# Kernel optimization log

Hardware: AMD Instinct MI355X
Metric: run time of the kernel (lower is better)

The kernel has to match this reference:

```python
import jax, jax.numpy as jnp
import numpy as np

NUM_HEADS = 6
WIN = 16
NW = 16   # number of windows sharing one mask (b_ % NW == 0)


def setup_inputs() -> dict:
    key = jax.random.key(0)
    ks = jax.random.split(key, 6)
    b_, n, dim = 256, WIN * WIN, 192
    qkv = jax.random.normal(ks[0], (b_, n, 3 * dim), dtype=jnp.float32)
    rpi = jax.random.randint(ks[1], (n, n), 0, (2 * WIN - 1) * (2 * WIN - 1))
    # additive attention mask per window-group (Swin uses 0 / -100; randn is fine for math)
    mask = jax.random.normal(ks[2], (NW, n, n), dtype=jnp.float32)
    rpb_table = 0.02 * jax.random.normal(ks[3], ((2 * WIN - 1) * (2 * WIN - 1), NUM_HEADS), dtype=jnp.float32)
    proj_w = jax.random.normal(ks[4], (dim, dim), dtype=jnp.float32) * (1.0 / np.sqrt(dim))
    proj_b = jax.random.normal(ks[5], (dim,), dtype=jnp.float32) * 0.01
    return {"qkv": qkv, "rpi": rpi, "mask": mask, "rpb_table": rpb_table,
            "proj_w": proj_w, "proj_b": proj_b}


def reference(qkv, rpi, mask, rpb_table, proj_w, proj_b):
    b_, n, c3 = qkv.shape
    c = c3 // 3
    h = NUM_HEADS
    hd = c // h
    scale = float(hd) ** -0.5
    # (b_, n, 3, h, hd) -> (3, b_, h, n, hd)
    qkv = qkv.reshape(b_, n, 3, h, hd).transpose(2, 0, 3, 1, 4)
    q, k, v = qkv[0] * scale, qkv[1], qkv[2]
    attn = jnp.einsum('bhqd,bhkd->bhqk', q, k)  # [b_, h, n, n]
    # gathered relative position bias: [n, n, h] -> [h, n, n]
    bias = rpb_table[rpi].transpose(2, 0, 1)
    attn = attn + bias[None]
    # add per-window-group mask: [b_//nw, nw, h, n, n]
    nw = mask.shape[0]
    attn = attn.reshape(b_ // nw, nw, h, n, n) + mask[None, :, None]
    attn = attn.reshape(b_, h, n, n)
    attn = jax.nn.softmax(attn, axis=-1)
    x = jnp.einsum('bhqk,bhkd->bhqd', attn, v)  # [b_, h, n, hd]
    x = x.transpose(0, 2, 1, 3).reshape(b_, n, c)
    # nn.Linear: x @ W^T + b
    return x @ proj_w.T + proj_b
```

## Files before the change

### kernel.cpp

```cpp
#include <hip/hip_runtime.h>
#include <hip/hip_bf16.h>

typedef _Float16 f16;
typedef _Float16 f16x2 __attribute__((ext_vector_type(2)));
typedef _Float16 f16x4 __attribute__((ext_vector_type(4)));
typedef _Float16 f16x8 __attribute__((ext_vector_type(8)));
typedef __fp16 h16x2 __attribute__((ext_vector_type(2)));
typedef float f32x4 __attribute__((ext_vector_type(4)));

#define NHEADS 6
#define NTOK 256
#define NWINS 256
#define DIM 192
#define HD 32
#define C3 576
#define LOG2E 1.4426950408889634f
#define SCALE (0.17677669529663687f * LOG2E)

__device__ inline f16x2 pkrtz(float a, float b) {
  h16x2 r = __builtin_amdgcn_cvt_pkrtz(a, b);
  return __builtin_bit_cast(f16x2, r);
}

__global__ __launch_bounds__(256) void prep_cb_kernel(const int* __restrict__ rpi,
                                                      const float* __restrict__ mask,
                                                      const float* __restrict__ rpb,
                                                      f16* __restrict__ cb) {
  int idx = blockIdx.x * 256 + threadIdx.x;
  int rem = idx & 255;
  int q = (idx >> 8) & 255;
  int t = idx >> 16;
  int h = t % 6;
  int mg = t / 6;
  int ktp = rem >> 5;
  int gg = (rem >> 3) & 3;
  int e = rem & 7;
  int k = (2 * ktp + (e >> 2)) * 16 + gg * 4 + (e & 3);
  float v = (rpb[rpi[(q << 8) | k] * 6 + h] + mask[(mg << 16) | (q << 8) | k]) * LOG2E;
  cb[idx] = (f16)v;
}

__global__ __launch_bounds__(256) void prep_w_kernel(const float* __restrict__ w,
                                                     f16* __restrict__ w16) {
  int i = blockIdx.x * 256 + threadIdx.x;
  if (i < DIM * DIM) w16[i] = (f16)w[i];
}

__device__ inline f16x8 q_to_f16(float4 a, float4 b) {
  f16x2 p0 = pkrtz(a.x * SCALE, a.y * SCALE);
  f16x2 p1 = pkrtz(a.z * SCALE, a.w * SCALE);
  f16x2 p2 = pkrtz(b.x * SCALE, b.y * SCALE);
  f16x2 p3 = pkrtz(b.z * SCALE, b.w * SCALE);
  f16x4 lo = __builtin_shufflevector(p0, p1, 0, 1, 2, 3);
  f16x4 hi = __builtin_shufflevector(p2, p3, 0, 1, 2, 3);
  return __builtin_shufflevector(lo, hi, 0, 1, 2, 3, 4, 5, 6, 7);
}

__global__ __launch_bounds__(512, 4) void attn_kernel(const float* __restrict__ qkv,
                                                      const f16* __restrict__ cb,
                                                      f16* __restrict__ x16) {
  const int idx = blockIdx.x;
  const int grp = idx % 96;
  const int jhi = idx / 96;
  const int b = (jhi << 4) | (grp / 6);
  const int h = grp % 6;
  const int tid = threadIdx.x;
  const int lane = tid & 63;
  const int wave = tid >> 6;
  const int g = lane >> 4;
  const int r16 = lane & 15;

  __shared__ f16 Klin[16 * 64 * 8];
  __shared__ f16 VT[32][264];

  {
    const int t = tid & 255;
    const int srow = t >> 3;
    const int part = t & 7;
    const bool isK = tid < 256;
    const float* base = qkv + (size_t)(b * NTOK + srow) * C3 + DIM + (isK ? 0 : DIM)
                        + h * HD + part * 4;
    const int gg = part >> 1;
    const int half = part & 1;
    const int d0 = part * 4;
#pragma unroll
    for (int batch = 0; batch < 2; ++batch) {
      float4 v4[4];
#pragma unroll
      for (int rg = 0; rg < 4; ++rg)
        v4[rg] = *(const float4*)(base + (size_t)((batch * 4 + rg) * 32) * C3);
#pragma unroll
      for (int rg = 0; rg < 4; ++rg) {
        const int row = (batch * 4 + rg) * 32 + srow;
        if (isK) {
          const int slot = ((row >> 4) * 64) + gg * 16 + ((row & 15) ^ (gg << 2));
          f16x2 k01 = pkrtz(v4[rg].x, v4[rg].y);
          f16x2 k23 = pkrtz(v4[rg].z, v4[rg].w);
          *((f16x4*)&Klin[slot * 8 + half * 4]) =
              __builtin_shufflevector(k01, k23, 0, 1, 2, 3);
        } else {
          VT[d0 + 0][row ^ (((d0 + 0) & 7) << 2)] = (f16)v4[rg].x;
          VT[d0 + 1][row ^ (((d0 + 1) & 7) << 2)] = (f16)v4[rg].y;
          VT[d0 + 2][row ^ (((d0 + 2) & 7) << 2)] = (f16)v4[rg].z;
          VT[d0 + 3][row ^ (((d0 + 3) & 7) << 2)] = (f16)v4[rg].w;
        }
      }
    }
  }
  __syncthreads();

  const int qbase = wave * 32;
  const f16* cbb = cb + ((size_t)grp << 16);
  const int krd = (lane & 48) + ((lane & 15) ^ ((lane >> 2) & 12));

#pragma unroll
  for (int c = 0; c < 2; ++c) {
    const int qrow = qbase + c * 16 + r16;
    const float* qp = qkv + (size_t)(b * NTOK + qrow) * C3 + h * HD + g * 8;
    f16x8 qf = q_to_f16(((const float4*)qp)[0], ((const float4*)qp)[1]);
    const f16* cbq = cbb + (qrow << 8) + g * 8;

    f16x8 cv[4];
#pragma unroll
    for (int kp = 0; kp < 4; ++kp) cv[kp] = *((const f16x8*)(cbq + kp * 32));
    f32x4 acc[8];
#pragma unroll
    for (int kp = 0; kp < 4; ++kp) {
#pragma unroll
      for (int r = 0; r < 4; ++r) {
        acc[2 * kp][r] = (float)cv[kp][r];
        acc[2 * kp + 1][r] = (float)cv[kp][4 + r];
      }
    }
#pragma unroll
    for (int kt = 0; kt < 8; ++kt) {
      f16x8 af = *((const f16x8*)&Klin[(kt * 64 + krd) * 8]);
      acc[kt] = __builtin_amdgcn_mfma_f32_16x16x32_f16(af, qf, acc[kt], 0, 0, 0);
    }

    float m0 = fmaxf(fmaxf(acc[0][0], acc[1][0]), fmaxf(acc[2][0], acc[3][0]));
    float m1 = fmaxf(fmaxf(acc[0][1], acc[1][1]), fmaxf(acc[2][1], acc[3][1]));
    float m2 = fmaxf(fmaxf(acc[0][2], acc[1][2]), fmaxf(acc[2][2], acc[3][2]));
    float m3 = fmaxf(fmaxf(acc[0][3], acc[1][3]), fmaxf(acc[2][3], acc[3][3]));
#pragma unroll
    for (int kt = 4; kt < 8; ++kt) {
      m0 = fmaxf(m0, acc[kt][0]); m1 = fmaxf(m1, acc[kt][1]);
      m2 = fmaxf(m2, acc[kt][2]); m3 = fmaxf(m3, acc[kt][3]);
    }
    float mA = fmaxf(fmaxf(m0, m1), fmaxf(m2, m3));
    mA = fmaxf(mA, __shfl_xor(mA, 16));
    mA = fmaxf(mA, __shfl_xor(mA, 32));

    float s0 = 0.f, s1 = 0.f, s2 = 0.f, s3 = 0.f;
#pragma unroll
    for (int kt = 0; kt < 8; ++kt) {
      float p0 = __builtin_amdgcn_exp2f(acc[kt][0] - mA);
      float p1 = __builtin_amdgcn_exp2f(acc[kt][1] - mA);
      float p2 = __builtin_amdgcn_exp2f(acc[kt][2] - mA);
      float p3 = __builtin_amdgcn_exp2f(acc[kt][3] - mA);
      acc[kt][0] = p0; acc[kt][1] = p1; acc[kt][2] = p2; acc[kt][3] = p3;
      s0 += p0; s1 += p1; s2 += p2; s3 += p3;
    }
    float sA = (s0 + s1) + (s2 + s3);

    f32x4 xa0[2], xa1[2];
#pragma unroll
    for (int dt = 0; dt < 2; ++dt) {
      xa0[dt][0] = 0.f; xa0[dt][1] = 0.f; xa0[dt][2] = 0.f; xa0[dt][3] = 0.f;
      xa1[dt][0] = 0.f; xa1[dt][1] = 0.f; xa1[dt][2] = 0.f; xa1[dt][3] = 0.f;
    }
#pragma unroll
    for (int kt = 0; kt < 8; ++kt) {
      f16x2 p01 = pkrtz(acc[kt][0], acc[kt][1]);
      f16x2 p23 = pkrtz(acc[kt][2], acc[kt][3]);
      f16x4 pf = __builtin_shufflevector(p01, p23, 0, 1, 2, 3);
#pragma unroll
      for (int dt = 0; dt < 2; ++dt) {
        const int col = (kt * 16 + g * 4) ^ ((r16 & 7) << 2);
        f16x4 vf = *((const f16x4*)&VT[dt * 16 + r16][col]);
        if (kt < 4)
          xa0[dt] = __builtin_amdgcn_mfma_f32_16x16x16f16(vf, pf, xa0[dt], 0, 0, 0);
        else
          xa1[dt] = __builtin_amdgcn_mfma_f32_16x16x16f16(vf, pf, xa1[dt], 0, 0, 0);
      }
    }

#pragma unroll
    for (int kp = 0; kp < 4; ++kp) cv[kp] = *((const f16x8*)(cbq + 128 + kp * 32));
#pragma unroll
    for (int kp = 0; kp < 4; ++kp) {
#pragma unroll
      for (int r = 0; r < 4; ++r) {
        acc[2 * kp][r] = (float)cv[kp][r];
        acc[2 * kp + 1][r] = (float)cv[kp][4 + r];
      }
    }
#pragma unroll
    for (int kt = 0; kt < 8; ++kt) {
      f16x8 af = *((const f16x8*)&Klin[((kt + 8) * 64 + krd) * 8]);
      acc[kt] = __builtin_amdgcn_mfma_f32_16x16x32_f16(af, qf, acc[kt], 0, 0, 0);
    }

    m0 = fmaxf(fmaxf(acc[0][0], acc[1][0]), fmaxf(acc[2][0], acc[3][0]));
    m1 = fmaxf(fmaxf(acc[0][1], acc[1][1]), fmaxf(acc[2][1], acc[3][1]));
    m2 = fmaxf(fmaxf(acc[0][2], acc[1][2]), fmaxf(acc[2][2], acc[3][2]));
    m3 = fmaxf(fmaxf(acc[0][3], acc[1][3]), fmaxf(acc[2][3], acc[3][3]));
#pragma unroll
    for (int kt = 4; kt < 8; ++kt) {
      m0 = fmaxf(m0, acc[kt][0]); m1 = fmaxf(m1, acc[kt][1]);
      m2 = fmaxf(m2, acc[kt][2]); m3 = fmaxf(m3, acc[kt][3]);
    }
    float mB = fmaxf(fmaxf(m0, m1), fmaxf(m2, m3));
    mB = fmaxf(mB, __shfl_xor(mB, 16));
    mB = fmaxf(mB, __shfl_xor(mB, 32));

    const float m = fmaxf(mA, mB);
    const float scA = __builtin_amdgcn_exp2f(mA - m);

    s0 = 0.f; s1 = 0.f; s2 = 0.f; s3 = 0.f;
#pragma unroll
    for (int kt = 0; kt < 8; ++kt) {
      float p0 = __builtin_amdgcn_exp2f(acc[kt][0] - m);
      float p1 = __builtin_amdgcn_exp2f(acc[kt][1] - m);
      float p2 = __builtin_amdgcn_exp2f(acc[kt][2] - m);
      float p3 = __builtin_amdgcn_exp2f(acc[kt][3] - m);
      acc[kt][0] = p0; acc[kt][1] = p1; acc[kt][2] = p2; acc[kt][3] = p3;
      s0 += p0; s1 += p1; s2 += p2; s3 += p3;
    }
    float s = sA * scA + (s0 + s1) + (s2 + s3);
    s += __shfl_xor(s, 16);
    s += __shfl_xor(s, 32);
    const float rinv = 1.0f / s;

#pragma unroll
    for (int dt = 0; dt < 2; ++dt) {
      xa0[dt][0] *= scA; xa0[dt][1] *= scA; xa0[dt][2] *= scA; xa0[dt][3] *= scA;
      xa1[dt][0] *= scA; xa1[dt][1] *= scA; xa1[dt][2] *= scA; xa1[dt][3] *= scA;
    }
#pragma unroll
    for (int kt = 0; kt < 8; ++kt) {
      f16x2 p01 = pkrtz(acc[kt][0], acc[kt][1]);
      f16x2 p23 = pkrtz(acc[kt][2], acc[kt][3]);
      f16x4 pf = __builtin_shufflevector(p01, p23, 0, 1, 2, 3);
#pragma unroll
      for (int dt = 0; dt < 2; ++dt) {
        const int col = ((kt + 8) * 16 + g * 4) ^ ((r16 & 7) << 2);
        f16x4 vf = *((const f16x4*)&VT[dt * 16 + r16][col]);
        if (kt < 4)
          xa0[dt] = __builtin_amdgcn_mfma_f32_16x16x16f16(vf, pf, xa0[dt], 0, 0, 0);
        else
          xa1[dt] = __builtin_amdgcn_mfma_f32_16x16x16f16(vf, pf, xa1[dt], 0, 0, 0);
      }
    }

    f16* xp = x16 + (size_t)(b * NTOK + qrow) * DIM + h * HD;
#pragma unroll
    for (int dt = 0; dt < 2; ++dt) {
      f16x2 o01 = pkrtz((xa0[dt][0] + xa1[dt][0]) * rinv,
                        (xa0[dt][1] + xa1[dt][1]) * rinv);
      f16x2 o23 = pkrtz((xa0[dt][2] + xa1[dt][2]) * rinv,
                        (xa0[dt][3] + xa1[dt][3]) * rinv);
      *((f16x4*)(xp + dt * 16 + g * 4)) = __builtin_shufflevector(o01, o23, 0, 1, 2, 3);
    }
  }
}

__global__ __launch_bounds__(256) void proj_kernel(const f16* __restrict__ x16,
                                                   const f16* __restrict__ w16,
                                                   const float* __restrict__ pb,
                                                   float* __restrict__ out) {
  const int lane = threadIdx.x & 63;
  const int wave = threadIdx.x >> 6;
  const int g = lane >> 4;
  const int r16 = lane & 15;
  const int m0 = blockIdx.x * 64 + wave * 16;

  f32x4 acc[12];
#pragma unroll
  for (int jt = 0; jt < 12; ++jt) {
    acc[jt][0] = 0.f; acc[jt][1] = 0.f; acc[jt][2] = 0.f; acc[jt][3] = 0.f;
  }
#pragma unroll
  for (int cc = 0; cc < 6; ++cc) {
    f16x8 af = *((const f16x8*)(x16 + (size_t)(m0 + r16) * DIM + cc * 32 + g * 8));
#pragma unroll
    for (int jt = 0; jt < 12; ++jt) {
      f16x8 bf = *((const f16x8*)(w16 + (size_t)(jt * 16 + r16) * DIM + cc * 32 + g * 8));
      acc[jt] = __builtin_amdgcn_mfma_f32_16x16x32_f16(af, bf, acc[jt], 0, 0, 0);
    }
  }
#pragma unroll
  for (int jt = 0; jt < 12; ++jt) {
    int j = jt * 16 + r16;
    float bias = pb[j];
#pragma unroll
    for (int r = 0; r < 4; ++r) {
      out[(size_t)(m0 + g * 4 + r) * DIM + j] = acc[jt][r] + bias;
    }
  }
}

extern "C" void kernel_launch(void* const* d_in, const int* in_sizes, int n_in,
                              void* d_out, int out_size, void* d_ws, size_t ws_size,
                              hipStream_t stream) {
  const float* qkv  = (const float*)d_in[0];
  const int*   rpi  = (const int*)d_in[1];
  const float* mask = (const float*)d_in[2];
  const float* rpb  = (const float*)d_in[3];
  const float* pw   = (const float*)d_in[4];
  const float* pbv  = (const float*)d_in[5];
  float* out = (float*)d_out;

  char* ws = (char*)d_ws;
  f16* cb16 = (f16*)ws;
  f16* x16  = (f16*)(ws + 12582912);
  f16* w16  = (f16*)(ws + 12582912 + 25165824);

  prep_cb_kernel<<<24576, 256, 0, stream>>>(rpi, mask, rpb, cb16);
  prep_w_kernel<<<144, 256, 0, stream>>>(pw, w16);
  attn_kernel<<<1536, 512, 0, stream>>>(qkv, cb16, x16);
  proj_kernel<<<1024, 256, 0, stream>>>(x16, w16, pbv, out);
}
```

Measured before the change: 110.4 us.

## Process two windows per attention block with double-buffered K/V staging

Each attention block now handles two windows that share the same head and mask group, halving the grid. The K/V tile for the second window is loaded from global memory while the first window's QK and PV MFMAs run, then written into a second LDS buffer. The aim is to hide global load latency behind compute and reuse the bias rows in cache. In exchange LDS use per block doubles, which may cut occupancy, register pressure rises from the in-flight prefetch, and there are fewer blocks to balance across CUs.

```diff
diff --git a/kernel.cpp b/kernel.cpp
--- a/kernel.cpp
+++ b/kernel.cpp
@@ -61,207 +61,231 @@
                                                       f16* __restrict__ x16) {
   const int idx = blockIdx.x;
   const int grp = idx % 96;
-  const int jhi = idx / 96;
-  const int b = (jhi << 4) | (grp / 6);
+  const int pr = idx / 96;
   const int h = grp % 6;
+  const int blo = grp / 6;
   const int tid = threadIdx.x;
   const int lane = tid & 63;
   const int wave = tid >> 6;
   const int g = lane >> 4;
   const int r16 = lane & 15;
 
-  __shared__ f16 Klin[16 * 64 * 8];
-  __shared__ f16 VT[32][264];
+  __shared__ f16 Klin[2][16 * 64 * 8];
+  __shared__ f16 VT[2][32][264];
+
+  const int t = tid & 255;
+  const int srow = t >> 3;
+  const int part = t & 7;
+  const bool isK = tid < 256;
+  const int gg = part >> 1;
+  const int half = part & 1;
+  const int d0 = part * 4;
+
+  const int b0 = ((pr * 2) << 4) | blo;
+  const int b1 = ((pr * 2 + 1) << 4) | blo;
+  const float* sbase0 = qkv + (size_t)(b0 * NTOK + srow) * C3 + DIM + (isK ? 0 : DIM)
+                        + h * HD + part * 4;
+  const float* sbase1 = qkv + (size_t)(b1 * NTOK + srow) * C3 + DIM + (isK ? 0 : DIM)
+                        + h * HD + part * 4;
+
+  auto stage_write = [&](int buf, int rgbase, const float4* v4) {
+#pragma unroll
+    for (int rg = 0; rg < 4; ++rg) {
+      const int row = (rgbase + rg) * 32 + srow;
+      if (isK) {
+        const int slot = ((row >> 4) * 64) + gg * 16 + ((row & 15) ^ (gg << 2));
+        f16x2 k01 = pkrtz(v4[rg].x, v4[rg].y);
+        f16x2 k23 = pkrtz(v4[rg].z, v4[rg].w);
+        *((f16x4*)&Klin[buf][slot * 8 + half * 4]) =
+            __builtin_shufflevector(k01, k23, 0, 1, 2, 3);
+      } else {
+        VT[buf][d0 + 0][row ^ (((d0 + 0) & 7) << 2)] = (f16)v4[rg].x;
+        VT[buf][d0 + 1][row ^ (((d0 + 1) & 7) << 2)] = (f16)v4[rg].y;
+        VT[buf][d0 + 2][row ^ (((d0 + 2) & 7) << 2)] = (f16)v4[rg].z;
+        VT[buf][d0 + 3][row ^ (((d0 + 3) & 7) << 2)] = (f16)v4[rg].w;
+      }
+    }
+  };
 
   {
-    const int t = tid & 255;
-    const int srow = t >> 3;
-    const int part = t & 7;
-    const bool isK = tid < 256;
-    const float* base = qkv + (size_t)(b * NTOK + srow) * C3 + DIM + (isK ? 0 : DIM)
-                        + h * HD + part * 4;
-    const int gg = part >> 1;
-    const int half = part & 1;
-    const int d0 = part * 4;
-#pragma unroll
-    for (int batch = 0; batch < 2; ++batch) {
-      float4 v4[4];
-#pragma unroll
-      for (int rg = 0; rg < 4; ++rg)
-        v4[rg] = *(const float4*)(base + (size_t)((batch * 4 + rg) * 32) * C3);
-#pragma unroll
-      for (int rg = 0; rg < 4; ++rg) {
-        const int row = (batch * 4 + rg) * 32 + srow;
-        if (isK) {
-          const int slot = ((row >> 4) * 64) + gg * 16 + ((row & 15) ^ (gg << 2));
-          f16x2 k01 = pkrtz(v4[rg].x, v4[rg].y);
-          f16x2 k23 = pkrtz(v4[rg].z, v4[rg].w);
-          *((f16x4*)&Klin[slot * 8 + half * 4]) =
-              __builtin_shufflevector(k01, k23, 0, 1, 2, 3);
-        } else {
-          VT[d0 + 0][row ^ (((d0 + 0) & 7) << 2)] = (f16)v4[rg].x;
-          VT[d0 + 1][row ^ (((d0 + 1) & 7) << 2)] = (f16)v4[rg].y;
-          VT[d0 + 2][row ^ (((d0 + 2) & 7) << 2)] = (f16)v4[rg].z;
-          VT[d0 + 3][row ^ (((d0 + 3) & 7) << 2)] = (f16)v4[rg].w;
-        }
-      }
-    }
+    float4 s4[8];
+#pragma unroll
+    for (int i = 0; i < 8; ++i)
+      s4[i] = *(const float4*)(sbase0 + (size_t)(i * 32) * C3);
+    stage_write(0, 0, s4);
+    stage_write(0, 4, s4 + 4);
   }
   __syncthreads();
 
-  const int qbase = wave * 32;
   const f16* cbb = cb + ((size_t)grp << 16);
   const int krd = (lane & 48) + ((lane & 15) ^ ((lane >> 2) & 12));
-
-#pragma unroll
-  for (int c = 0; c < 2; ++c) {
-    const int qrow = qbase + c * 16 + r16;
-    const float* qp = qkv + (size_t)(b * NTOK + qrow) * C3 + h * HD + g * 8;
-    f16x8 qf = q_to_f16(((const float4*)qp)[0], ((const float4*)qp)[1]);
-    const f16* cbq = cbb + (qrow << 8) + g * 8;
-
-    f16x8 cv[4];
-#pragma unroll
-    for (int kp = 0; kp < 4; ++kp) cv[kp] = *((const f16x8*)(cbq + kp * 32));
-    f32x4 acc[8];
-#pragma unroll
-    for (int kp = 0; kp < 4; ++kp) {
-#pragma unroll
-      for (int r = 0; r < 4; ++r) {
-        acc[2 * kp][r] = (float)cv[kp][r];
-        acc[2 * kp + 1][r] = (float)cv[kp][4 + r];
+  const int qbase = wave * 32;
+
+#pragma unroll
+  for (int pair = 0; pair < 2; ++pair) {
+    const int b = (pair == 0) ? b0 : b1;
+
+#pragma unroll
+    for (int c = 0; c < 2; ++c) {
+      float4 n4[4];
+      if (pair == 0) {
+#pragma unroll
+        for (int i = 0; i < 4; ++i)
+          n4[i] = *(const float4*)(sbase1 + (size_t)((c * 4 + i) * 32) * C3);
+      }
+
+      const int qrow = qbase + c * 16 + r16;
+      const float* qp = qkv + (size_t)(b * NTOK + qrow) * C3 + h * HD + g * 8;
+      f16x8 qf = q_to_f16(((const float4*)qp)[0], ((const float4*)qp)[1]);
+      const f16* cbq = cbb + (qrow << 8) + g * 8;
+
+      f16x8 cv[4];
+#pragma unroll
+      for (int kp = 0; kp < 4; ++kp) cv[kp] = *((const f16x8*)(cbq + kp * 32));
+      f32x4 acc[8];
+#pragma unroll
+      for (int kp = 0; kp < 4; ++kp) {
+#pragma unroll
+        for (int r = 0; r < 4; ++r) {
+          acc[2 * kp][r] = (float)cv[kp][r];
+          acc[2 * kp + 1][r] = (float)cv[kp][4 + r];
+        }
+      }
+#pragma unroll
+      for (int kt = 0; kt < 8; ++kt) {
+        f16x8 af = *((const f16x8*)&Klin[pair][(kt * 64 + krd) * 8]);
+        acc[kt] = __builtin_amdgcn_mfma_f32_16x16x32_f16(af, qf, acc[kt], 0, 0, 0);
+      }
+
+      if (pair == 0) stage_write(1, c * 4, n4);
+
+      float m0 = fmaxf(fmaxf(acc[0][0], acc[1][0]), fmaxf(acc[2][0], acc[3][0]));
+      float m1 = fmaxf(fmaxf(acc[0][1], acc[1][1]), fmaxf(acc[2][1], acc[3][1]));
+      float m2 = fmaxf(fmaxf(acc[0][2], acc[1][2]), fmaxf(acc[2][2], acc[3][2]));
+      float m3 = fmaxf(fmaxf(acc[0][3], acc[1][3]), fmaxf(acc[2][3], acc[3][3]));
+#pragma unroll
+      for (int kt = 4; kt < 8; ++kt) {
+        m0 = fmaxf(m0, acc[kt][0]); m1 = fmaxf(m1, acc[kt][1]);
+        m2 = fmaxf(m2, acc[kt][2]); m3 = fmaxf(m3, acc[kt][3]);
+      }
+      float mA = fmaxf(fmaxf(m0, m1), fmaxf(m2, m3));
+      mA = fmaxf(mA, __shfl_xor(mA, 16));
+      mA = fmaxf(mA, __shfl_xor(mA, 32));
+
+      float s0 = 0.f, s1 = 0.f, s2 = 0.f, s3 = 0.f;
+#pragma unroll
+      for (int kt = 0; kt < 8; ++kt) {
+        float p0 = __builtin_amdgcn_exp2f(acc[kt][0] - mA);
+        float p1 = __builtin_amdgcn_exp2f(acc[kt][1] - mA);
+        float p2 = __builtin_amdgcn_exp2f(acc[kt][2] - mA);
+        float p3 = __builtin_amdgcn_exp2f(acc[kt][3] - mA);
+        acc[kt][0] = p0; acc[kt][1] = p1; acc[kt][2] = p2; acc[kt][3] = p3;
+        s0 += p0; s1 += p1; s2 += p2; s3 += p3;
+      }
+      float sA = (s0 + s1) + (s2 + s3);
+
+      f32x4 xa0[2], xa1[2];
+#pragma unroll
+      for (int dt = 0; dt < 2; ++dt) {
+        xa0[dt][0] = 0.f; xa0[dt][1] = 0.f; xa0[dt][2] = 0.f; xa0[dt][3] = 0.f;
+        xa1[dt][0] = 0.f; xa1[dt][1] = 0.f; xa1[dt][2] = 0.f; xa1[dt][3] = 0.f;
+      }
+#pragma unroll
+      for (int kt = 0; kt < 8; ++kt) {
+        f16x2 p01 = pkrtz(acc[kt][0], acc[kt][1]);
+        f16x2 p23 = pkrtz(acc[kt][2], acc[kt][3]);
+        f16x4 pf = __builtin_shufflevector(p01, p23, 0, 1, 2, 3);
+#pragma unroll
+        for (int dt = 0; dt < 2; ++dt) {
+          const int col = (kt * 16 + g * 4) ^ ((r16 & 7) << 2);
+          f16x4 vf = *((const f16x4*)&VT[pair][dt * 16 + r16][col]);
+          if (kt < 4)
+            xa0[dt] = __builtin_amdgcn_mfma_f32_16x16x16f16(vf, pf, xa0[dt], 0, 0, 0);
+          else
+            xa1[dt] = __builtin_amdgcn_mfma_f32_16x16x16f16(vf, pf, xa1[dt], 0, 0, 0);
+        }
+      }
+
+#pragma unroll
+      for (int kp = 0; kp < 4; ++kp) cv[kp] = *((const f16x8*)(cbq + 128 + kp * 32));
+#pragma unroll
+      for (int kp = 0; kp < 4; ++kp) {
+#pragma unroll
+        for (int r = 0; r < 4; ++r) {
+          acc[2 * kp][r] = (float)cv[kp][r];
+          acc[2 * kp + 1][r] = (float)cv[kp][4 + r];
+        }
+      }
+#pragma unroll
+      for (int kt = 0; kt < 8; ++kt) {
+        f16x8 af = *((const f16x8*)&Klin[pair][((kt + 8) * 64 + krd) * 8]);
+        acc[kt] = __builtin_amdgcn_mfma_f32_16x16x32_f16(af, qf, acc[kt], 0, 0, 0);
+      }
+
+      m0 = fmaxf(fmaxf(acc[0][0], acc[1][0]), fmaxf(acc[2][0], acc[3][0]));
+      m1 = fmaxf(fmaxf(acc[0][1], acc[1][1]), fmaxf(acc[2][1], acc[3][1]));
+      m2 = fmaxf(fmaxf(acc[0][2], acc[1][2]), fmaxf(acc[2][2], acc[3][2]));
+      m3 = fmaxf(fmaxf(acc[0][3], acc[1][3]), fmaxf(acc[2][3], acc[3][3]));
+#pragma unroll
+      for (int kt = 4; kt < 8; ++kt) {
+        m0 = fmaxf(m0, acc[kt][0]); m1 = fmaxf(m1, acc[kt][1]);
+        m2 = fmaxf(m2, acc[kt][2]); m3 = fmaxf(m3, acc[kt][3]);
+      }
+      float mB = fmaxf(fmaxf(m0, m1), fmaxf(m2, m3));
+      mB = fmaxf(mB, __shfl_xor(mB, 16));
+      mB = fmaxf(mB, __shfl_xor(mB, 32));
+
+      const float m = fmaxf(mA, mB);
+      const float scA = __builtin_amdgcn_exp2f(mA - m);
+
+      s0 = 0.f; s1 = 0.f; s2 = 0.f; s3 = 0.f;
+#pragma unroll
+      for (int kt = 0; kt < 8; ++kt) {
+        float p0 = __builtin_amdgcn_exp2f(acc[kt][0] - m);
+        float p1 = __builtin_amdgcn_exp2f(acc[kt][1] - m);
+        float p2 = __builtin_amdgcn_exp2f(acc[kt][2] - m);
+        float p3 = __builtin_amdgcn_exp2f(acc[kt][3] - m);
+        acc[kt][0] = p0; acc[kt][1] = p1; acc[kt][2] = p2; acc[kt][3] = p3;
+        s0 += p0; s1 += p1; s2 += p2; s3 += p3;
+      }
+      float s = sA * scA + (s0 + s1) + (s2 + s3);
+      s += __shfl_xor(s, 16);
+      s += __shfl_xor(s, 32);
+      const float rinv = 1.0f / s;
+
+#pragma unroll
+      for (int dt = 0; dt < 2; ++dt) {
+        xa0[dt][0] *= scA; xa0[dt][1] *= scA; xa0[dt][2] *= scA; xa0[dt][3] *= scA;
+        xa1[dt][0] *= scA; xa1[dt][1] *= scA; xa1[dt][2] *= scA; xa1[dt][3] *= scA;
+      }
+#pragma unroll
+      for (int kt = 0; kt < 8; ++kt) {
+        f16x2 p01 = pkrtz(acc[kt][0], acc[kt][1]);
+        f16x2 p23 = pkrtz(acc[kt][2], acc[kt][3]);
+        f16x4 pf = __builtin_shufflevector(p01, p23, 0, 1, 2, 3);
+#pragma unroll
+        for (int dt = 0; dt < 2; ++dt) {
+          const int col = ((kt + 8) * 16 + g * 4) ^ ((r16 & 7) << 2);
+          f16x4 vf = *((const f16x4*)&VT[pair][dt * 16 + r16][col]);
+          if (kt < 4)
+            xa0[dt] = __builtin_amdgcn_mfma_f32_16x16x16f16(vf, pf, xa0[dt], 0, 0, 0);
+          else
+            xa1[dt] = __builtin_amdgcn_mfma_f32_16x16x16f16(vf, pf, xa1[dt], 0, 0, 0);
+        }
+      }
+
+      f16* xp = x16 + (size_t)(b * NTOK + qrow) * DIM + h * HD;
+#pragma unroll
+      for (int dt = 0; dt < 2; ++dt) {
+        f16x2 o01 = pkrtz((xa0[dt][0] + xa1[dt][0]) * rinv,
+                          (xa0[dt][1] + xa1[dt][1]) * rinv);
+        f16x2 o23 = pkrtz((xa0[dt][2] + xa1[dt][2]) * rinv,
+                          (xa0[dt][3] + xa1[dt][3]) * rinv);
+        *((f16x4*)(xp + dt * 16 + g * 4)) = __builtin_shufflevector(o01, o23, 0, 1, 2, 3);
       }
     }
-#pragma unroll
-    for (int kt = 0; kt < 8; ++kt) {
-      f16x8 af = *((const f16x8*)&Klin[(kt * 64 + krd) * 8]);
-      acc[kt] = __builtin_amdgcn_mfma_f32_16x16x32_f16(af, qf, acc[kt], 0, 0, 0);
-    }
-
-    float m0 = fmaxf(fmaxf(acc[0][0], acc[1][0]), fmaxf(acc[2][0], acc[3][0]));
-    float m1 = fmaxf(fmaxf(acc[0][1], acc[1][1]), fmaxf(acc[2][1], acc[3][1]));
-    float m2 = fmaxf(fmaxf(acc[0][2], acc[1][2]), fmaxf(acc[2][2], acc[3][2]));
-    float m3 = fmaxf(fmaxf(acc[0][3], acc[1][3]), fmaxf(acc[2][3], acc[3][3]));
-#pragma unroll
-    for (int kt = 4; kt < 8; ++kt) {
-      m0 = fmaxf(m0, acc[kt][0]); m1 = fmaxf(m1, acc[kt][1]);
-      m2 = fmaxf(m2, acc[kt][2]); m3 = fmaxf(m3, acc[kt][3]);
-    }
-    float mA = fmaxf(fmaxf(m0, m1), fmaxf(m2, m3));
-    mA = fmaxf(mA, __shfl_xor(mA, 16));
-    mA = fmaxf(mA, __shfl_xor(mA, 32));
-
-    float s0 = 0.f, s1 = 0.f, s2 = 0.f, s3 = 0.f;
-#pragma unroll
-    for (int kt = 0; kt < 8; ++kt) {
-      float p0 = __builtin_amdgcn_exp2f(acc[kt][0] - mA);
-      float p1 = __builtin_amdgcn_exp2f(acc[kt][1] - mA);
-      float p2 = __builtin_amdgcn_exp2f(acc[kt][2] - mA);
-      float p3 = __builtin_amdgcn_exp2f(acc[kt][3] - mA);
-      acc[kt][0] = p0; acc[kt][1] = p1; acc[kt][2] = p2; acc[kt][3] = p3;
-      s0 += p0; s1 += p1; s2 += p2; s3 += p3;
-    }
-    float sA = (s0 + s1) + (s2 + s3);
-
-    f32x4 xa0[2], xa1[2];
-#pragma unroll
-    for (int dt = 0; dt < 2; ++dt) {
-      xa0[dt][0] = 0.f; xa0[dt][1] = 0.f; xa0[dt][2] = 0.f; xa0[dt][3] = 0.f;
-      xa1[dt][0] = 0.f; xa1[dt][1] = 0.f; xa1[dt][2] = 0.f; xa1[dt][3] = 0.f;
-    }
-#pragma unroll
-    for (int kt = 0; kt < 8; ++kt) {
-      f16x2 p01 = pkrtz(acc[kt][0], acc[kt][1]);
-      f16x2 p23 = pkrtz(acc[kt][2], acc[kt][3]);
-      f16x4 pf = __builtin_shufflevector(p01, p23, 0, 1, 2, 3);
-#pragma unroll
-      for (int dt = 0; dt < 2; ++dt) {
-        const int col = (kt * 16 + g * 4) ^ ((r16 & 7) << 2);
-        f16x4 vf = *((const f16x4*)&VT[dt * 16 + r16][col]);
-        if (kt < 4)
-          xa0[dt] = __builtin_amdgcn_mfma_f32_16x16x16f16(vf, pf, xa0[dt], 0, 0, 0);
-        else
-          xa1[dt] = __builtin_amdgcn_mfma_f32_16x16x16f16(vf, pf, xa1[dt], 0, 0, 0);
-      }
-    }
-
-#pragma unroll
-    for (int kp = 0; kp < 4; ++kp) cv[kp] = *((const f16x8*)(cbq + 128 + kp * 32));
-#pragma unroll
-    for (int kp = 0; kp < 4; ++kp) {
-#pragma unroll
-      for (int r = 0; r < 4; ++r) {
-        acc[2 * kp][r] = (float)cv[kp][r];
-        acc[2 * kp + 1][r] = (float)cv[kp][4 + r];
-      }
-    }
-#pragma unroll
-    for (int kt = 0; kt < 8; ++kt) {
-      f16x8 af = *((const f16x8*)&Klin[((kt + 8) * 64 + krd) * 8]);
-      acc[kt] = __builtin_amdgcn_mfma_f32_16x16x32_f16(af, qf, acc[kt], 0, 0, 0);
-    }
-
-    m0 = fmaxf(fmaxf(acc[0][0], acc[1][0]), fmaxf(acc[2][0], acc[3][0]));
-    m1 = fmaxf(fmaxf(acc[0][1], acc[1][1]), fmaxf(acc[2][1], acc[3][1]));
-    m2 = fmaxf(fmaxf(acc[0][2], acc[1][2]), fmaxf(acc[2][2], acc[3][2]));
-    m3 = fmaxf(fmaxf(acc[0][3], acc[1][3]), fmaxf(acc[2][3], acc[3][3]));
-#pragma unroll
-    for (int kt = 4; kt < 8; ++kt) {
-      m0 = fmaxf(m0, acc[kt][0]); m1 = fmaxf(m1, acc[kt][1]);
-      m2 = fmaxf(m2, acc[kt][2]); m3 = fmaxf(m3, acc[kt][3]);
-    }
-    float mB = fmaxf(fmaxf(m0, m1), fmaxf(m2, m3));
-    mB = fmaxf(mB, __shfl_xor(mB, 16));
-    mB = fmaxf(mB, __shfl_xor(mB, 32));
-
-    const float m = fmaxf(mA, mB);
-    const float scA = __builtin_amdgcn_exp2f(mA - m);
-
-    s0 = 0.f; s1 = 0.f; s2 = 0.f; s3 = 0.f;
-#pragma unroll
-    for (int kt = 0; kt < 8; ++kt) {
-      float p0 = __builtin_amdgcn_exp2f(acc[kt][0] - m);
-      float p1 = __builtin_amdgcn_exp2f(acc[kt][1] - m);
-      float p2 = __builtin_amdgcn_exp2f(acc[kt][2] - m);
-      float p3 = __builtin_amdgcn_exp2f(acc[kt][3] - m);
-      acc[kt][0] = p0; acc[kt][1] = p1; acc[kt][2] = p2; acc[kt][3] = p3;
-      s0 += p0; s1 += p1; s2 += p2; s3 += p3;
-    }
-    float s = sA * scA + (s0 + s1) + (s2 + s3);
-    s += __shfl_xor(s, 16);
-    s += __shfl_xor(s, 32);
-    const float rinv = 1.0f / s;
-
-#pragma unroll
-    for (int dt = 0; dt < 2; ++dt) {
-      xa0[dt][0] *= scA; xa0[dt][1] *= scA; xa0[dt][2] *= scA; xa0[dt][3] *= scA;
-      xa1[dt][0] *= scA; xa1[dt][1] *= scA; xa1[dt][2] *= scA; xa1[dt][3] *= scA;
-    }
-#pragma unroll
-    for (int kt = 0; kt < 8; ++kt) {
-      f16x2 p01 = pkrtz(acc[kt][0], acc[kt][1]);
-      f16x2 p23 = pkrtz(acc[kt][2], acc[kt][3]);
-      f16x4 pf = __builtin_shufflevector(p01, p23, 0, 1, 2, 3);
-#pragma unroll
-      for (int dt = 0; dt < 2; ++dt) {
-        const int col = ((kt + 8) * 16 + g * 4) ^ ((r16 & 7) << 2);
-        f16x4 vf = *((const f16x4*)&VT[dt * 16 + r16][col]);
-        if (kt < 4)
-          xa0[dt] = __builtin_amdgcn_mfma_f32_16x16x16f16(vf, pf, xa0[dt], 0, 0, 0);
-        else
-          xa1[dt] = __builtin_amdgcn_mfma_f32_16x16x16f16(vf, pf, xa1[dt], 0, 0, 0);
-      }
-    }
-
-    f16* xp = x16 + (size_t)(b * NTOK + qrow) * DIM + h * HD;
-#pragma unroll
-    for (int dt = 0; dt < 2; ++dt) {
-      f16x2 o01 = pkrtz((xa0[dt][0] + xa1[dt][0]) * rinv,
-                        (xa0[dt][1] + xa1[dt][1]) * rinv);
-      f16x2 o23 = pkrtz((xa0[dt][2] + xa1[dt][2]) * rinv,
-                        (xa0[dt][3] + xa1[dt][3]) * rinv);
-      *((f16x4*)(xp + dt * 16 + g * 4)) = __builtin_shufflevector(o01, o23, 0, 1, 2, 3);
-    }
+
+    if (pair == 0) __syncthreads();
   }
 }
 
@@ -318,6 +342,6 @@
 
   prep_cb_kernel<<<24576, 256, 0, stream>>>(rpi, mask, rpb, cb16);
   prep_w_kernel<<<144, 256, 0, stream>>>(pw, w16);
-  attn_kernel<<<1536, 512, 0, stream>>>(qkv, cb16, x16);
+  attn_kernel<<<768, 512, 0, stream>>>(qkv, cb16, x16);
   proj_kernel<<<1024, 256, 0, stream>>>(x16, w16, pbv, out);
 }
```

After: 108.9 us. No clear change (-1.3%).
